# Optimization experiments

Measured on AMD Instinct MI355X. Metric: run time of the kernel, lower is better.

## Reference

```python
import jax, jax.numpy as jnp
import numpy as np

NUM_TRACKS = [5313, 1643, 128, 0]
MAX_TRACKS = max(NUM_TRACKS)
EMBED_DIM = 1536
LN_EPS = 1e-5


def setup_inputs() -> dict:
    key = jax.random.key(0)
    ks = jax.random.split(key, 8)
    B, S, D = 4, 896, EMBED_DIM
    inp = {
        "x": jax.random.normal(ks[0], (B, S, D), dtype=jnp.float32),
        "head_idx": jax.random.randint(ks[1], (B,), 0, 4, dtype=jnp.int64) if jax.config.jax_enable_x64 else jax.random.randint(ks[1], (B,), 0, 4).astype(jnp.int32),
    }
    for i, n in enumerate([5313, 1643, 128]):
        inp[f"gamma{i}"] = jnp.ones((D,), jnp.float32)
        inp[f"beta{i}"] = jnp.zeros((D,), jnp.float32)
        inp[f"W{i}"] = jax.random.normal(ks[2 + i], (n, D), dtype=jnp.float32) * 0.02
        inp[f"b{i}"] = jnp.zeros((n,), jnp.float32)
    return inp


def _linear_head(x, gamma, beta, W, b):
    # LayerNormFP32 -> Linear -> softplus, cast back to orig dtype
    orig_dtype = x.dtype
    xf = x.astype(jnp.float32)
    mu = jnp.mean(xf, axis=-1, keepdims=True)
    var = jnp.var(xf, axis=-1, keepdims=True)  # biased, as torch LayerNorm
    xn = (xf - mu) * jax.lax.rsqrt(var + LN_EPS) * gamma + beta
    h = jax.nn.softplus(jnp.einsum("bsd,td->bst", xn, W) + b)
    return h.astype(orig_dtype)


def reference(x, head_idx, gamma0, beta0, W0, b0,
              gamma1, beta1, W1, b1, gamma2, beta2, W2, b2):
    params = [(gamma0, beta0, W0, b0),
              (gamma1, beta1, W1, b1),
              (gamma2, beta2, W2, b2),
              None]  # ZeroHead
    B, S, _ = x.shape
    logits = jnp.zeros((B, S, MAX_TRACKS), dtype=x.dtype)
    for i, p in enumerate(params):
        if p is None:
            padded = jnp.zeros((B, S, MAX_TRACKS), dtype=x.dtype)
        else:
            h = _linear_head(x, *p)  # [B, S, n_i]
            pad = MAX_TRACKS - h.shape[-1]
            padded = jnp.pad(h, ((0, 0), (0, 0), (0, pad))) if pad > 0 else h
        mask = (head_idx == i)[:, None, None]
        logits = jnp.where(mask, padded, logits)
    return logits
```

## Files before the change

### kernel.cpp

```cpp
#include <hip/hip_runtime.h>
#include <hip/hip_bf16.h>

#define EMBED 1536
#define SEQ   896
#define NOUT  5313

#define N0 5313
#define N1 1643
#define N2 128
#define W0OFF 0
#define W1OFF 5376
#define W2OFF 7040
#define PTOT  7168

typedef __attribute__((ext_vector_type(8))) short bf16x8;
typedef __attribute__((ext_vector_type(4))) float f32x4;

__device__ __forceinline__ void gload_lds16(const void* g, void* l) {
    __builtin_amdgcn_global_load_lds(
        (const __attribute__((address_space(1))) void*)g,
        (__attribute__((address_space(3))) void*)l, 16, 0, 0);
}

__global__ __launch_bounds__(128) void ln_kernel(
    const float* __restrict__ x, const int* __restrict__ head_idx,
    const float* __restrict__ g0, const float* __restrict__ be0,
    const float* __restrict__ g1, const float* __restrict__ be1,
    const float* __restrict__ g2, const float* __restrict__ be2,
    __hip_bfloat16* __restrict__ xn)
{
    const int row = blockIdx.x;
    const int b = row / SEQ;
    const int h = head_idx[b];
    const float* gamma = (h == 1) ? g1 : (h == 2) ? g2 : g0;
    const float* beta  = (h == 1) ? be1 : (h == 2) ? be2 : be0;
    const float* xr = x + (size_t)row * EMBED;
    const int tid = threadIdx.x;

    float4 v[3];
    float sum = 0.f, sq = 0.f;
#pragma unroll
    for (int i = 0; i < 3; ++i) {
        v[i] = ((const float4*)xr)[tid + i * 128];
        sum += v[i].x + v[i].y + v[i].z + v[i].w;
        sq  += v[i].x * v[i].x + v[i].y * v[i].y + v[i].z * v[i].z + v[i].w * v[i].w;
    }
#pragma unroll
    for (int off = 32; off > 0; off >>= 1) {
        sum += __shfl_down(sum, off);
        sq  += __shfl_down(sq, off);
    }
    __shared__ float s_sum[2], s_sq[2];
    const int wave = tid >> 6, lane = tid & 63;
    if (lane == 0) { s_sum[wave] = sum; s_sq[wave] = sq; }
    __syncthreads();
    const float mu  = (s_sum[0] + s_sum[1]) * (1.f / EMBED);
    const float var = (s_sq[0] + s_sq[1]) * (1.f / EMBED) - mu * mu;
    const float rs  = rsqrtf(var + 1e-5f);

    __hip_bfloat16* xo = xn + (size_t)row * EMBED;
#pragma unroll
    for (int i = 0; i < 3; ++i) {
        const int idx = tid + i * 128;
        float4 gv = ((const float4*)gamma)[idx];
        float4 bv = ((const float4*)beta)[idx];
        union { __hip_bfloat16 h4[4]; short4 s4; } u;
        u.h4[0] = __float2bfloat16((v[i].x - mu) * rs * gv.x + bv.x);
        u.h4[1] = __float2bfloat16((v[i].y - mu) * rs * gv.y + bv.y);
        u.h4[2] = __float2bfloat16((v[i].z - mu) * rs * gv.z + bv.z);
        u.h4[3] = __float2bfloat16((v[i].w - mu) * rs * gv.w + bv.w);
        ((short4*)xo)[idx] = u.s4;
    }
}

__global__ __launch_bounds__(256) void wconv_kernel(
    const float* __restrict__ W0, const float* __restrict__ W1,
    const float* __restrict__ W2, __hip_bfloat16* __restrict__ wpad)
{
    const int gid = blockIdx.x * 256 + threadIdx.x;
    const int r = gid / 192;
    const int c = (gid - r * 192) * 8;
    const float* src = nullptr;
    if (r < W1OFF)      { if (r < N0) src = W0 + (size_t)r * EMBED; }
    else if (r < W2OFF) { int rr = r - W1OFF; if (rr < N1) src = W1 + (size_t)rr * EMBED; }
    else                { int rr = r - W2OFF; if (rr < N2) src = W2 + (size_t)rr * EMBED; }
    union { __hip_bfloat16 h8[8]; int4 v4; } u;
    if (src) {
        float4 a = ((const float4*)(src + c))[0];
        float4 b = ((const float4*)(src + c))[1];
        u.h8[0] = __float2bfloat16(a.x); u.h8[1] = __float2bfloat16(a.y);
        u.h8[2] = __float2bfloat16(a.z); u.h8[3] = __float2bfloat16(a.w);
        u.h8[4] = __float2bfloat16(b.x); u.h8[5] = __float2bfloat16(b.y);
        u.h8[6] = __float2bfloat16(b.z); u.h8[7] = __float2bfloat16(b.w);
    } else {
        u.v4 = make_int4(0, 0, 0, 0);
    }
    *(int4*)(wpad + (size_t)r * EMBED + c) = u.v4;
}

__global__ __launch_bounds__(256) void biasconv_kernel(
    const float* __restrict__ b0, const float* __restrict__ b1,
    const float* __restrict__ b2, float* __restrict__ bpad)
{
    const int i = blockIdx.x * 256 + threadIdx.x;
    float v = 0.f;
    if (i < W1OFF)      { if (i < N0) v = b0[i]; }
    else if (i < W2OFF) { int j = i - W1OFF; if (j < N1) v = b1[j]; }
    else                { int j = i - W2OFF; if (j < N2) v = b2[j]; }
    bpad[i] = v;
}

__global__ __launch_bounds__(256, 2) void head_gemm(
    const __hip_bfloat16* __restrict__ xn,
    const __hip_bfloat16* __restrict__ wpad,
    const float* __restrict__ bpad,
    const int* __restrict__ head_idx,
    float* __restrict__ out)
{
    const int nt = blockIdx.x, mt = blockIdx.y, b = blockIdx.z;
    const int h = head_idx[b];
    int nrows, wbase;
    if (h == 0)      { nrows = N0; wbase = W0OFF; }
    else if (h == 1) { nrows = N1; wbase = W1OFF; }
    else if (h == 2) { nrows = N2; wbase = W2OFF; }
    else             { nrows = 0;  wbase = 0; }

    const int tid = threadIdx.x;
    const int col0 = nt * 128;
    float* outb = out + ((size_t)b * SEQ + (size_t)mt * 128) * NOUT;

    if (col0 >= nrows) {
        for (int i = tid; i < 128 * 128; i += 256) {
            const int r = i >> 7;
            const int cc = col0 + (i & 127);
            if (cc < NOUT) outb[(size_t)r * NOUT + cc] = 0.f;
        }
        return;
    }

    __shared__ __hip_bfloat16 As[128 * 64];
    __shared__ __hip_bfloat16 Bs[128 * 64];
    const __hip_bfloat16* Ab = xn + ((size_t)b * SEQ + (size_t)mt * 128) * EMBED;
    const __hip_bfloat16* Bb = wpad + (size_t)(wbase + col0) * EMBED;

    const int wave = tid >> 6, lane = tid & 63;
    const int wm = wave >> 1, wn = wave & 1;
    const int fm = lane & 15, quad = lane >> 4;
    const int fsw = fm & 7;

    f32x4 acc[4][4] = {};

    for (int kt = 0; kt < EMBED / 64; ++kt) {
        const int k0 = kt * 64;
        __syncthreads();
#pragma unroll
        for (int i = 0; i < 4; ++i) {
            const int c = tid + i * 256;
            const int arow = c >> 3;
            const int kc = (c & 7) ^ (arow & 7);
            gload_lds16(Ab + (size_t)arow * EMBED + k0 + kc * 8, As + c * 8);
        }
#pragma unroll
        for (int i = 0; i < 4; ++i) {
            const int c = tid + i * 256;
            const int brow = c >> 3;
            const int kc = (c & 7) ^ (brow & 7);
            gload_lds16(Bb + (size_t)brow * EMBED + k0 + kc * 8, Bs + c * 8);
        }
        __syncthreads();
#pragma unroll
        for (int ks = 0; ks < 2; ++ks) {
            bf16x8 af[4], bfr[4];
#pragma unroll
            for (int i = 0; i < 4; ++i)
                af[i] = *(const bf16x8*)&As[(wm * 64 + i * 16 + fm) * 64 +
                                            (((ks << 2) + quad) ^ fsw) * 8];
#pragma unroll
            for (int j = 0; j < 4; ++j)
                bfr[j] = *(const bf16x8*)&Bs[(wn * 64 + j * 16 + fm) * 64 +
                                             (((ks << 2) + quad) ^ fsw) * 8];
#pragma unroll
            for (int i = 0; i < 4; ++i)
#pragma unroll
                for (int j = 0; j < 4; ++j)
                    acc[i][j] = __builtin_amdgcn_mfma_f32_16x16x32_bf16(
                        af[i], bfr[j], acc[i][j], 0, 0, 0);
        }
    }

#pragma unroll
    for (int j = 0; j < 4; ++j) {
        const int lcol = col0 + wn * 64 + j * 16 + fm;
        const bool inb = lcol < NOUT;
        const bool valid = lcol < nrows;
        const float bv = valid ? bpad[wbase + lcol] : 0.f;
#pragma unroll
        for (int i = 0; i < 4; ++i) {
            const int rbase = wm * 64 + i * 16 + quad * 4;
#pragma unroll
            for (int r = 0; r < 4; ++r) {
                if (!inb) continue;
                const float v = acc[i][j][r] + bv;
                const float sp = fmaxf(v, 0.f) + __logf(1.f + __expf(-fabsf(v)));
                outb[(size_t)(rbase + r) * NOUT + lcol] = valid ? sp : 0.f;
            }
        }
    }
}

extern "C" void kernel_launch(void* const* d_in, const int* in_sizes, int n_in,
                              void* d_out, int out_size, void* d_ws, size_t ws_size,
                              hipStream_t stream) {
    const float* x   = (const float*)d_in[0];
    const int* hidx  = (const int*)d_in[1];
    const float* g0  = (const float*)d_in[2];
    const float* be0 = (const float*)d_in[3];
    const float* W0  = (const float*)d_in[4];
    const float* b0  = (const float*)d_in[5];
    const float* g1  = (const float*)d_in[6];
    const float* be1 = (const float*)d_in[7];
    const float* W1  = (const float*)d_in[8];
    const float* b1  = (const float*)d_in[9];
    const float* g2  = (const float*)d_in[10];
    const float* be2 = (const float*)d_in[11];
    const float* W2  = (const float*)d_in[12];
    const float* b2  = (const float*)d_in[13];
    float* out = (float*)d_out;

    const size_t XN_BYTES   = (size_t)4 * SEQ * EMBED * 2;
    const size_t WPAD_BYTES = (size_t)PTOT * EMBED * 2;
    __hip_bfloat16* xn   = (__hip_bfloat16*)d_ws;
    __hip_bfloat16* wpad = (__hip_bfloat16*)((char*)d_ws + XN_BYTES);
    float* bpad          = (float*)((char*)d_ws + XN_BYTES + WPAD_BYTES);

    ln_kernel<<<4 * SEQ, 128, 0, stream>>>(x, hidx, g0, be0, g1, be1, g2, be2, xn);
    wconv_kernel<<<(PTOT * 192) / 256, 256, 0, stream>>>(W0, W1, W2, wpad);
    biasconv_kernel<<<PTOT / 256, 256, 0, stream>>>(b0, b1, b2, bpad);
    dim3 grid(42, 7, 4);
    head_gemm<<<grid, 256, 0, stream>>>(xn, wpad, bpad, hidx, out);
}
```

Before: 194.9 us.

## Fuse prep kernels and skip weight conversion for unused heads

Merges the layernorm and weight-conversion kernels into one launch and drops the bias padding kernel, reading bias directly in the GEMM epilogue. Weight regions not selected by any batch's head index are no longer converted, and layernorm rows for the zero head are skipped. The GEMM grid is flattened with batch as the fastest index to interleave work across batches. Padding semantics in the epilogue are kept via the valid mask.

```diff
diff --git a/kernel.cpp b/kernel.cpp
--- a/kernel.cpp
+++ b/kernel.cpp
@@ -13,6 +13,9 @@
 #define W2OFF 7040
 #define PTOT  7168
 
+#define LN_BLOCKS 1792
+#define WC_BLOCKS 5376
+
 typedef __attribute__((ext_vector_type(8))) short bf16x8;
 typedef __attribute__((ext_vector_type(4))) float f32x4;
 
@@ -22,102 +25,106 @@
         (__attribute__((address_space(3))) void*)l, 16, 0, 0);
 }
 
-__global__ __launch_bounds__(128) void ln_kernel(
+__global__ __launch_bounds__(256) void prep_kernel(
     const float* __restrict__ x, const int* __restrict__ head_idx,
     const float* __restrict__ g0, const float* __restrict__ be0,
     const float* __restrict__ g1, const float* __restrict__ be1,
     const float* __restrict__ g2, const float* __restrict__ be2,
-    __hip_bfloat16* __restrict__ xn)
+    const float* __restrict__ W0, const float* __restrict__ W1,
+    const float* __restrict__ W2,
+    __hip_bfloat16* __restrict__ xn, __hip_bfloat16* __restrict__ wpad)
 {
-    const int row = blockIdx.x;
-    const int b = row / SEQ;
-    const int h = head_idx[b];
-    const float* gamma = (h == 1) ? g1 : (h == 2) ? g2 : g0;
-    const float* beta  = (h == 1) ? be1 : (h == 2) ? be2 : be0;
-    const float* xr = x + (size_t)row * EMBED;
     const int tid = threadIdx.x;
 
-    float4 v[3];
-    float sum = 0.f, sq = 0.f;
-#pragma unroll
-    for (int i = 0; i < 3; ++i) {
-        v[i] = ((const float4*)xr)[tid + i * 128];
-        sum += v[i].x + v[i].y + v[i].z + v[i].w;
-        sq  += v[i].x * v[i].x + v[i].y * v[i].y + v[i].z * v[i].z + v[i].w * v[i].w;
-    }
-#pragma unroll
-    for (int off = 32; off > 0; off >>= 1) {
-        sum += __shfl_down(sum, off);
-        sq  += __shfl_down(sq, off);
-    }
-    __shared__ float s_sum[2], s_sq[2];
-    const int wave = tid >> 6, lane = tid & 63;
-    if (lane == 0) { s_sum[wave] = sum; s_sq[wave] = sq; }
-    __syncthreads();
-    const float mu  = (s_sum[0] + s_sum[1]) * (1.f / EMBED);
-    const float var = (s_sq[0] + s_sq[1]) * (1.f / EMBED) - mu * mu;
-    const float rs  = rsqrtf(var + 1e-5f);
-
-    __hip_bfloat16* xo = xn + (size_t)row * EMBED;
-#pragma unroll
-    for (int i = 0; i < 3; ++i) {
-        const int idx = tid + i * 128;
-        float4 gv = ((const float4*)gamma)[idx];
-        float4 bv = ((const float4*)beta)[idx];
-        union { __hip_bfloat16 h4[4]; short4 s4; } u;
-        u.h4[0] = __float2bfloat16((v[i].x - mu) * rs * gv.x + bv.x);
-        u.h4[1] = __float2bfloat16((v[i].y - mu) * rs * gv.y + bv.y);
-        u.h4[2] = __float2bfloat16((v[i].z - mu) * rs * gv.z + bv.z);
-        u.h4[3] = __float2bfloat16((v[i].w - mu) * rs * gv.w + bv.w);
-        ((short4*)xo)[idx] = u.s4;
-    }
-}
-
-__global__ __launch_bounds__(256) void wconv_kernel(
-    const float* __restrict__ W0, const float* __restrict__ W1,
-    const float* __restrict__ W2, __hip_bfloat16* __restrict__ wpad)
-{
-    const int gid = blockIdx.x * 256 + threadIdx.x;
-    const int r = gid / 192;
-    const int c = (gid - r * 192) * 8;
-    const float* src = nullptr;
-    if (r < W1OFF)      { if (r < N0) src = W0 + (size_t)r * EMBED; }
-    else if (r < W2OFF) { int rr = r - W1OFF; if (rr < N1) src = W1 + (size_t)rr * EMBED; }
-    else                { int rr = r - W2OFF; if (rr < N2) src = W2 + (size_t)rr * EMBED; }
-    union { __hip_bfloat16 h8[8]; int4 v4; } u;
-    if (src) {
-        float4 a = ((const float4*)(src + c))[0];
-        float4 b = ((const float4*)(src + c))[1];
-        u.h8[0] = __float2bfloat16(a.x); u.h8[1] = __float2bfloat16(a.y);
-        u.h8[2] = __float2bfloat16(a.z); u.h8[3] = __float2bfloat16(a.w);
-        u.h8[4] = __float2bfloat16(b.x); u.h8[5] = __float2bfloat16(b.y);
-        u.h8[6] = __float2bfloat16(b.z); u.h8[7] = __float2bfloat16(b.w);
+    if (blockIdx.x < LN_BLOCKS) {
+        const int half = tid >> 7;
+        const int lt   = tid & 127;
+        const int row  = blockIdx.x * 2 + half;
+        const int b    = row / SEQ;
+        const int h    = head_idx[b];
+        if (h == 3) return;
+
+        const float* gamma = (h == 1) ? g1 : (h == 2) ? g2 : g0;
+        const float* beta  = (h == 1) ? be1 : (h == 2) ? be2 : be0;
+        const float* xr = x + (size_t)row * EMBED;
+
+        float4 v[3];
+        float sum = 0.f, sq = 0.f;
+#pragma unroll
+        for (int i = 0; i < 3; ++i) {
+            v[i] = ((const float4*)xr)[lt + i * 128];
+            sum += v[i].x + v[i].y + v[i].z + v[i].w;
+            sq  += v[i].x * v[i].x + v[i].y * v[i].y + v[i].z * v[i].z + v[i].w * v[i].w;
+        }
+#pragma unroll
+        for (int off = 32; off > 0; off >>= 1) {
+            sum += __shfl_down(sum, off);
+            sq  += __shfl_down(sq, off);
+        }
+        __shared__ float s_sum[4], s_sq[4];
+        const int wave = tid >> 6, lane = tid & 63;
+        if (lane == 0) { s_sum[wave] = sum; s_sq[wave] = sq; }
+        __syncthreads();
+        const int wb = half << 1;
+        const float mu  = (s_sum[wb] + s_sum[wb + 1]) * (1.f / EMBED);
+        const float var = (s_sq[wb] + s_sq[wb + 1]) * (1.f / EMBED) - mu * mu;
+        const float rs  = rsqrtf(var + 1e-5f);
+
+        __hip_bfloat16* xo = xn + (size_t)row * EMBED;
+#pragma unroll
+        for (int i = 0; i < 3; ++i) {
+            const int idx = lt + i * 128;
+            float4 gv = ((const float4*)gamma)[idx];
+            float4 bv = ((const float4*)beta)[idx];
+            union { __hip_bfloat16 h4[4]; short4 s4; } u;
+            u.h4[0] = __float2bfloat16((v[i].x - mu) * rs * gv.x + bv.x);
+            u.h4[1] = __float2bfloat16((v[i].y - mu) * rs * gv.y + bv.y);
+            u.h4[2] = __float2bfloat16((v[i].z - mu) * rs * gv.z + bv.z);
+            u.h4[3] = __float2bfloat16((v[i].w - mu) * rs * gv.w + bv.w);
+            ((short4*)xo)[idx] = u.s4;
+        }
     } else {
-        u.v4 = make_int4(0, 0, 0, 0);
-    }
-    *(int4*)(wpad + (size_t)r * EMBED + c) = u.v4;
-}
-
-__global__ __launch_bounds__(256) void biasconv_kernel(
-    const float* __restrict__ b0, const float* __restrict__ b1,
-    const float* __restrict__ b2, float* __restrict__ bpad)
-{
-    const int i = blockIdx.x * 256 + threadIdx.x;
-    float v = 0.f;
-    if (i < W1OFF)      { if (i < N0) v = b0[i]; }
-    else if (i < W2OFF) { int j = i - W1OFF; if (j < N1) v = b1[j]; }
-    else                { int j = i - W2OFF; if (j < N2) v = b2[j]; }
-    bpad[i] = v;
+        const int gid = (blockIdx.x - LN_BLOCKS) * 256 + tid;
+        const int r = gid / 192;
+        const int c = (gid - r * 192) * 8;
+        const int region = (r < W1OFF) ? 0 : (r < W2OFF) ? 1 : 2;
+        const int h0 = head_idx[0], h1 = head_idx[1];
+        const int h2 = head_idx[2], h3 = head_idx[3];
+        if (region != h0 && region != h1 && region != h2 && region != h3)
+            return;
+        const float* src = nullptr;
+        if (region == 0)      { if (r < N0) src = W0 + (size_t)r * EMBED; }
+        else if (region == 1) { int rr = r - W1OFF; if (rr < N1) src = W1 + (size_t)rr * EMBED; }
+        else                  { int rr = r - W2OFF; if (rr < N2) src = W2 + (size_t)rr * EMBED; }
+        union { __hip_bfloat16 h8[8]; int4 v4; } u;
+        if (src) {
+            float4 a = ((const float4*)(src + c))[0];
+            float4 b = ((const float4*)(src + c))[1];
+            u.h8[0] = __float2bfloat16(a.x); u.h8[1] = __float2bfloat16(a.y);
+            u.h8[2] = __float2bfloat16(a.z); u.h8[3] = __float2bfloat16(a.w);
+            u.h8[4] = __float2bfloat16(b.x); u.h8[5] = __float2bfloat16(b.y);
+            u.h8[6] = __float2bfloat16(b.z); u.h8[7] = __float2bfloat16(b.w);
+        } else {
+            u.v4 = make_int4(0, 0, 0, 0);
+        }
+        *(int4*)(wpad + (size_t)r * EMBED + c) = u.v4;
+    }
 }
 
 __global__ __launch_bounds__(256, 2) void head_gemm(
     const __hip_bfloat16* __restrict__ xn,
     const __hip_bfloat16* __restrict__ wpad,
-    const float* __restrict__ bpad,
+    const float* __restrict__ b0, const float* __restrict__ b1,
+    const float* __restrict__ b2,
     const int* __restrict__ head_idx,
     float* __restrict__ out)
 {
-    const int nt = blockIdx.x, mt = blockIdx.y, b = blockIdx.z;
+    const int id = blockIdx.x;
+    const int b  = id & 3;
+    const int t  = id >> 2;
+    const int mt = t % 7;
+    const int nt = t / 7;
+
     const int h = head_idx[b];
     int nrows, wbase;
     if (h == 0)      { nrows = N0; wbase = W0OFF; }
@@ -188,12 +195,13 @@
         }
     }
 
+    const float* bias = (h == 1) ? b1 : (h == 2) ? b2 : b0;
 #pragma unroll
     for (int j = 0; j < 4; ++j) {
         const int lcol = col0 + wn * 64 + j * 16 + fm;
         const bool inb = lcol < NOUT;
         const bool valid = lcol < nrows;
-        const float bv = valid ? bpad[wbase + lcol] : 0.f;
+        const float bv = valid ? bias[lcol] : 0.f;
 #pragma unroll
         for (int i = 0; i < 4; ++i) {
             const int rbase = wm * 64 + i * 16 + quad * 4;
@@ -227,15 +235,11 @@
     const float* b2  = (const float*)d_in[13];
     float* out = (float*)d_out;
 
-    const size_t XN_BYTES   = (size_t)4 * SEQ * EMBED * 2;
-    const size_t WPAD_BYTES = (size_t)PTOT * EMBED * 2;
+    const size_t XN_BYTES = (size_t)4 * SEQ * EMBED * 2;
     __hip_bfloat16* xn   = (__hip_bfloat16*)d_ws;
     __hip_bfloat16* wpad = (__hip_bfloat16*)((char*)d_ws + XN_BYTES);
-    float* bpad          = (float*)((char*)d_ws + XN_BYTES + WPAD_BYTES);
-
-    ln_kernel<<<4 * SEQ, 128, 0, stream>>>(x, hidx, g0, be0, g1, be1, g2, be2, xn);
-    wconv_kernel<<<(PTOT * 192) / 256, 256, 0, stream>>>(W0, W1, W2, wpad);
-    biasconv_kernel<<<PTOT / 256, 256, 0, stream>>>(b0, b1, b2, bpad);
-    dim3 grid(42, 7, 4);
-    head_gemm<<<grid, 256, 0, stream>>>(xn, wpad, bpad, hidx, out);
-}
+
+    prep_kernel<<<LN_BLOCKS + WC_BLOCKS, 256, 0, stream>>>(
+        x, hidx, g0, be0, g1, be1, g2, be2, W0, W1, W2, xn, wpad);
+    head_gemm<<<1176, 256, 0, stream>>>(xn, wpad, b0, b1, b2, hidx, out);
+}
```

Measured after the change: 214.9 us. 1.1x slower.
